# Optimization experiments

Measured on AMD Instinct MI355X. Metric: run time of the kernel, lower is better.

Reference implementation:

```python
import jax, jax.numpy as jnp
import numpy as np

S, B, D, H = 2048, 2, 1024, 16
DK = D // H  # 64
SCALE = 1.0 / np.sqrt(DK)


def setup_inputs() -> dict:
    key = jax.random.key(0)
    ks = jax.random.split(key, 12)
    std = 0.02
    return {
        "query": jax.random.normal(ks[0], (S, B, D), jnp.float32),
        "key": jax.random.normal(ks[1], (S, B, D), jnp.float32),
        "value": jax.random.normal(ks[2], (S, B, D), jnp.float32),
        "wq": jax.random.normal(ks[3], (D, D), jnp.float32) * std,
        "bq": jnp.zeros((D,), jnp.float32),
        "wk": jax.random.normal(ks[4], (D, D), jnp.float32) * std,
        "bk": jnp.zeros((D,), jnp.float32),
        "wv": jax.random.normal(ks[5], (D, D), jnp.float32) * std,
        "bv": jnp.zeros((D,), jnp.float32),
        "wo": jax.random.normal(ks[6], (D, D), jnp.float32) * std,
        "bo": jnp.zeros((D,), jnp.float32),
    }


def _proj(x, w, b):
    # (s, b, d_model) -> (s, b, heads, d_k); nn.Linear uses x @ W^T + b
    y = x @ w.T + b
    return y.reshape(*x.shape[:-1], H, DK)


def reference(query, key, value, wq, bq, wk, bk, wv, bv, wo, bo):
    q = _proj(query, wq, bq)   # (s, b, h, d)
    k = _proj(key, wk, bk)
    v = _proj(value, wv, bv)
    scores = jnp.einsum("ibhd,jbhd->ijbh", q, k) * SCALE  # (s_q, s_k, b, h)
    attn = jax.nn.softmax(scores, axis=1)  # softmax over key axis (dim=1)
    # dropout is identity in eval/reference mode
    x = jnp.einsum("ijbh,jbhd->ibhd", attn, v)  # (s, b, h, d)
    x = x.reshape(S, B, D)
    return x @ wo.T + bo
```

## Files before the change

### kernel.cpp

```cpp
#include <hip/hip_runtime.h>
#include <hip/hip_bf16.h>

namespace {

constexpr int SEQ = 2048;
constexpr int NB  = 2;
constexpr int DM  = 1024;
constexpr int NHD = 16;
constexpr int DKH = 64;
constexpr int MROWS = SEQ * NB;
constexpr float SM_SCALE = 0.125f;
constexpr size_t HT = (size_t)NB * NHD * SEQ * DKH;

typedef short bf16x8 __attribute__((ext_vector_type(8)));
typedef short bf16x4 __attribute__((ext_vector_type(4)));
typedef float f32x4  __attribute__((ext_vector_type(4)));

__device__ inline short f2bf(float f) {
    __hip_bfloat16 h = __float2bfloat16(f);
    return *reinterpret_cast<short*>(&h);
}

__device__ inline unsigned perm_pack_bf16(float hi, float lo) {
    return __builtin_amdgcn_perm(__float_as_uint(hi), __float_as_uint(lo),
                                 0x07060302u);
}

__device__ inline void gload_lds16(const short* g, short* l) {
    __builtin_amdgcn_global_load_lds(
        (const __attribute__((address_space(1))) void*)g,
        (__attribute__((address_space(3))) void*)l, 16, 0, 0);
}

__device__ inline f32x4 mfma16x16x16(bf16x4 a, bf16x4 b, f32x4 c) {
#if __has_builtin(__builtin_amdgcn_mfma_f32_16x16x16bf16_1k)
    return __builtin_amdgcn_mfma_f32_16x16x16bf16_1k(a, b, c, 0, 0, 0);
#else
    f32x4 d;
    asm("v_mfma_f32_16x16x16_bf16 %0, %1, %2, %3"
        : "=v"(d) : "v"(a), "v"(b), "v"(c));
    return d;
#endif
}

__global__ __launch_bounds__(256)
void cast3_kernel(const float* __restrict__ q, const float* __restrict__ k,
                  const float* __restrict__ v, short* __restrict__ oq,
                  short* __restrict__ ok, short* __restrict__ ov)
{
    const int t = blockIdx.x * 256 + threadIdx.x;
    const float* s = blockIdx.y == 0 ? q : blockIdx.y == 1 ? k : v;
    short* d       = blockIdx.y == 0 ? oq : blockIdx.y == 1 ? ok : ov;
    const float4 a = ((const float4*)s)[2 * t];
    const float4 b = ((const float4*)s)[2 * t + 1];
    short r[8] = {f2bf(a.x), f2bf(a.y), f2bf(a.z), f2bf(a.w),
                  f2bf(b.x), f2bf(b.y), f2bf(b.z), f2bf(b.w)};
    *(bf16x8*)(d + 8 * (size_t)t) = *(bf16x8*)r;
}

__global__ __launch_bounds__(256)
void castW_kernel(const float* __restrict__ w0, const float* __restrict__ w1,
                  const float* __restrict__ w2, const float* __restrict__ w3,
                  short* __restrict__ o)
{
    const int t = blockIdx.x * 256 + threadIdx.x;
    const float* s = blockIdx.y == 0 ? w0 : blockIdx.y == 1 ? w1
                   : blockIdx.y == 2 ? w2 : w3;
    short* d = o + (size_t)blockIdx.y * (DM * DM);
    const float4 a = ((const float4*)s)[2 * t];
    const float4 b = ((const float4*)s)[2 * t + 1];
    short r[8] = {f2bf(a.x), f2bf(a.y), f2bf(a.z), f2bf(a.w),
                  f2bf(b.x), f2bf(b.y), f2bf(b.z), f2bf(b.w)};
    *(bf16x8*)(d + 8 * (size_t)t) = *(bf16x8*)r;
}

__global__ __launch_bounds__(256)
void gemm_qkv(const short* __restrict__ X0, const short* __restrict__ X1,
              const short* __restrict__ X2, const short* __restrict__ W,
              const float* __restrict__ b0, const float* __restrict__ b1,
              const float* __restrict__ b2, short* __restrict__ Yh)
{
    __shared__ short As[128 * 64];
    __shared__ short Bs[128 * 64];
    const int tid  = threadIdx.x;
    const int lane = tid & 63;
    const int wave = tid >> 6;
    const int i16  = lane & 15;
    const int quad = lane >> 4;

    const int c    = blockIdx.y * gridDim.x + blockIdx.x;
    const int xcd  = c & 7;
    const int idx  = c >> 3;
    const int m0   = (xcd * 4 + (idx & 3)) * 128;
    const int n0g  = (idx >> 2) * 128;

    const int R0   = (wave & 1) * 64;
    const int C0   = (wave >> 1) * 64;

    const int seg = n0g >> 10;
    const short* X = seg == 0 ? X0 : seg == 1 ? X1 : X2;

    const int srow = lane >> 3;
    const int ssl  = (lane & 7) ^ srow;

    const short* ag[4]; short* al[4];
    const short* bg[4]; short* bl[4];
    #pragma unroll
    for (int i = 0; i < 4; ++i) {
        const int row = i * 32 + wave * 8 + srow;
        ag[i] = X + (size_t)(m0 + row) * DM + ssl * 8;
        al[i] = &As[i * 2048 + wave * 512];
        bg[i] = W + (size_t)(n0g + row) * DM + ssl * 8;
        bl[i] = &Bs[i * 2048 + wave * 512];
    }

    int aoff[4][2], boff[4][2];
    #pragma unroll
    for (int rt = 0; rt < 4; ++rt)
        #pragma unroll
        for (int kc = 0; kc < 2; ++kc)
            aoff[rt][kc] = (R0 + rt * 16 + i16) * 64 +
                           (((kc * 4 + quad) ^ (i16 & 7)) * 8);
    #pragma unroll
    for (int ct = 0; ct < 4; ++ct)
        #pragma unroll
        for (int kc = 0; kc < 2; ++kc)
            boff[ct][kc] = (C0 + ct * 16 + i16) * 64 +
                           (((kc * 4 + quad) ^ (i16 & 7)) * 8);

    f32x4 acc[4][4];
    #pragma unroll
    for (int rt = 0; rt < 4; ++rt)
        #pragma unroll
        for (int ct = 0; ct < 4; ++ct) acc[rt][ct] = (f32x4){0.f, 0.f, 0.f, 0.f};

    for (int ks = 0; ks < 16; ++ks) {
        __syncthreads();
        #pragma unroll
        for (int i = 0; i < 4; ++i) gload_lds16(ag[i], al[i]);
        #pragma unroll
        for (int i = 0; i < 4; ++i) gload_lds16(bg[i], bl[i]);
        __syncthreads();

        #pragma unroll
        for (int kc = 0; kc < 2; ++kc) {
            bf16x8 af[4], bfr[4];
            #pragma unroll
            for (int rt = 0; rt < 4; ++rt) af[rt] = *(const bf16x8*)&As[aoff[rt][kc]];
            #pragma unroll
            for (int ct = 0; ct < 4; ++ct) bfr[ct] = *(const bf16x8*)&Bs[boff[ct][kc]];
            #pragma unroll
            for (int rt = 0; rt < 4; ++rt)
                #pragma unroll
                for (int ct = 0; ct < 4; ++ct)
                    acc[rt][ct] = __builtin_amdgcn_mfma_f32_16x16x32_bf16(
                        af[rt], bfr[ct], acc[rt][ct], 0, 0, 0);
        }
        #pragma unroll
        for (int i = 0; i < 4; ++i) { ag[i] += 64; bg[i] += 64; }
    }

    #pragma unroll
    for (int ct = 0; ct < 4; ++ct) {
        const int n = n0g + C0 + ct * 16 + i16;
        const int nn  = n & 1023;
        const int h = nn >> 6, dk = nn & 63;
        const float* bp = seg == 0 ? b0 : seg == 1 ? b1 : b2;
        const float bb = bp[nn];
        const float sc = seg == 0 ? SM_SCALE : 1.0f;
        short* dst = Yh + (size_t)seg * HT;
        #pragma unroll
        for (int rt = 0; rt < 4; ++rt)
            #pragma unroll
            for (int r = 0; r < 4; ++r) {
                const int m = m0 + R0 + rt * 16 + quad * 4 + r;
                const int s = m >> 1, b = m & 1;
                dst[((size_t)(b * NHD + h) * SEQ + s) * DKH + dk] =
                    f2bf((acc[rt][ct][r] + bb) * sc);
            }
    }
}

__global__ __launch_bounds__(256)
void gemm_out(const short* __restrict__ X, const short* __restrict__ W,
              const float* __restrict__ bias, float* __restrict__ Y)
{
    __shared__ short As[128 * 64];
    __shared__ short Bs[64 * 64];
    const int tid  = threadIdx.x;
    const int lane = tid & 63;
    const int wave = tid >> 6;
    const int i16  = lane & 15;
    const int quad = lane >> 4;

    const int c   = blockIdx.y * gridDim.x + blockIdx.x;
    const int xcd = c & 7;
    const int idx = c >> 3;
    const int m0  = (xcd * 4 + (idx & 3)) * 128;
    const int n0  = (idx >> 2) * 64;

    const int R0   = wave * 32;

    const int srow = lane >> 3;
    const int ssl  = (lane & 7) ^ srow;

    const short* ag[4]; short* al[4];
    const short* bg[2]; short* bl[2];
    #pragma unroll
    for (int i = 0; i < 4; ++i) {
        const int row = i * 32 + wave * 8 + srow;
        ag[i] = X + (size_t)(m0 + row) * DM + ssl * 8;
        al[i] = &As[i * 2048 + wave * 512];
    }
    #pragma unroll
    for (int i = 0; i < 2; ++i) {
        const int row = i * 32 + wave * 8 + srow;
        bg[i] = W + (size_t)(n0 + row) * DM + ssl * 8;
        bl[i] = &Bs[i * 2048 + wave * 512];
    }

    int aoff[2][2], boff[4][2];
    #pragma unroll
    for (int rt = 0; rt < 2; ++rt)
        #pragma unroll
        for (int kc = 0; kc < 2; ++kc)
            aoff[rt][kc] = (R0 + rt * 16 + i16) * 64 +
                           (((kc * 4 + quad) ^ (i16 & 7)) * 8);
    #pragma unroll
    for (int ct = 0; ct < 4; ++ct)
        #pragma unroll
        for (int kc = 0; kc < 2; ++kc)
            boff[ct][kc] = (ct * 16 + i16) * 64 +
                           (((kc * 4 + quad) ^ (i16 & 7)) * 8);

    f32x4 acc[2][4];
    #pragma unroll
    for (int rt = 0; rt < 2; ++rt)
        #pragma unroll
        for (int ct = 0; ct < 4; ++ct) acc[rt][ct] = (f32x4){0.f, 0.f, 0.f, 0.f};

    for (int ks = 0; ks < 16; ++ks) {
        __syncthreads();
        #pragma unroll
        for (int i = 0; i < 4; ++i) gload_lds16(ag[i], al[i]);
        #pragma unroll
        for (int i = 0; i < 2; ++i) gload_lds16(bg[i], bl[i]);
        __syncthreads();

        #pragma unroll
        for (int kc = 0; kc < 2; ++kc) {
            bf16x8 af[2], bfr[4];
            #pragma unroll
            for (int rt = 0; rt < 2; ++rt) af[rt] = *(const bf16x8*)&As[aoff[rt][kc]];
            #pragma unroll
            for (int ct = 0; ct < 4; ++ct) bfr[ct] = *(const bf16x8*)&Bs[boff[ct][kc]];
            #pragma unroll
            for (int rt = 0; rt < 2; ++rt)
                #pragma unroll
                for (int ct = 0; ct < 4; ++ct)
                    acc[rt][ct] = __builtin_amdgcn_mfma_f32_16x16x32_bf16(
                        af[rt], bfr[ct], acc[rt][ct], 0, 0, 0);
        }
        #pragma unroll
        for (int i = 0; i < 4; ++i) ag[i] += 64;
        #pragma unroll
        for (int i = 0; i < 2; ++i) bg[i] += 64;
    }

    #pragma unroll
    for (int ct = 0; ct < 4; ++ct) {
        const int n = n0 + ct * 16 + i16;
        const float bb = bias[n];
        #pragma unroll
        for (int rt = 0; rt < 2; ++rt)
            #pragma unroll
            for (int r = 0; r < 4; ++r) {
                const int m = m0 + R0 + rt * 16 + quad * 4 + r;
                Y[(size_t)m * DM + n] = acc[rt][ct][r] + bb;
            }
    }
}

__global__ __launch_bounds__(256)
void transpose_v(const short* __restrict__ V, short* __restrict__ Vt)
{
    __shared__ alignas(16) short tile[64][72];
    const int tid = threadIdx.x;
    const int s0  = blockIdx.x * 64;
    const int bh  = blockIdx.y;
    const int row = tid >> 2;
    const int c0  = (tid & 3) * 16;

    const short* src = V + ((size_t)bh * SEQ + s0 + row) * DKH + c0;
    *(bf16x8*)&tile[row][c0]     = *(const bf16x8*)src;
    *(bf16x8*)&tile[row][c0 + 8] = *(const bf16x8*)(src + 8);
    __syncthreads();

    alignas(16) short vals[16];
    #pragma unroll
    for (int i = 0; i < 16; ++i) vals[i] = tile[c0 + i][row];
    short* dst = Vt + ((size_t)bh * DKH + row) * SEQ + s0 + c0;
    *(bf16x8*)dst       = *(bf16x8*)&vals[0];
    *(bf16x8*)(dst + 8) = *(bf16x8*)&vals[8];
}

__global__ __launch_bounds__(512)
void attn_mfma3(const short* __restrict__ Qb, const short* __restrict__ Kb,
                const short* __restrict__ Vtb, short* __restrict__ Xa)
{
    __shared__ char smem[35328];
    float* Of = (float*)smem;
    float* Ls = (float*)(smem + 34816);

    const int tid  = threadIdx.x;
    const int lane = tid & 63;
    const int wave = tid >> 6;
    const int half = wave >> 2;
    const int w4   = wave & 3;
    const int i16  = lane & 15;
    const int quad = lane >> 4;

    const int c   = blockIdx.y * gridDim.x + blockIdx.x;
    const int xcd = c & 7;
    const int idx = c >> 3;
    const int bh  = xcd * 4 + (idx >> 4);
    const int r0  = (idx & 15) * 128;

    short* Ks = (short*)(smem + half * 8192);
    short* Vs = (short*)(smem + 16384 + half * 8192);

    bf16x8 qf[2][2];
    #pragma unroll
    for (int qt = 0; qt < 2; ++qt) {
        const short* qrow =
            Qb + ((size_t)bh * SEQ + r0 + w4 * 32 + qt * 16 + i16) * DKH;
        qf[qt][0] = *(const bf16x8*)(qrow + quad * 8);
        qf[qt][1] = *(const bf16x8*)(qrow + 32 + quad * 8);
    }

    f32x4 o[2][4];
    #pragma unroll
    for (int qt = 0; qt < 2; ++qt)
        #pragma unroll
        for (int dkt = 0; dkt < 4; ++dkt) o[qt][dkt] = (f32x4){0.f, 0.f, 0.f, 0.f};
    float lsum[2] = {0.f, 0.f};

    const int srow = lane >> 3;
    const int ssl  = (lane & 7) ^ srow;
    const short* kg[2]; short* kl[2];
    const short* vg[2]; short* vl[2];
    #pragma unroll
    for (int i = 0; i < 2; ++i) {
        const int row = i * 32 + w4 * 8 + srow;
        kg[i] = Kb  + (size_t)bh * SEQ * DKH +
                (size_t)(half * 1024 + row) * DKH + ssl * 8;
        kl[i] = &Ks[i * 2048 + w4 * 512];
        vg[i] = Vtb + (size_t)bh * DKH * SEQ + (size_t)row * SEQ +
                half * 1024 + ssl * 8;
        vl[i] = &Vs[i * 2048 + w4 * 512];
    }

    int koff[4][2];
    #pragma unroll
    for (int t = 0; t < 4; ++t)
        #pragma unroll
        for (int kc = 0; kc < 2; ++kc)
            koff[t][kc] = (t * 16 + i16) * 64 +
                          (((kc * 4 + quad) ^ (i16 & 7)) * 8);
    int voff[4][4];
    #pragma unroll
    for (int jw = 0; jw < 4; ++jw)
        #pragma unroll
        for (int dkt = 0; dkt < 4; ++dkt)
            voff[jw][dkt] = (dkt * 16 + i16) * 64 +
                            (((2 * jw + (quad >> 1)) ^ (i16 & 7)) * 8) +
                            (quad & 1) * 4;

    for (int jt = 0; jt < 16; ++jt) {
        __syncthreads();
        gload_lds16(kg[0] + (size_t)jt * 64 * DKH, kl[0]);
        gload_lds16(kg[1] + (size_t)jt * 64 * DKH, kl[1]);
        gload_lds16(vg[0] + jt * 64, vl[0]);
        gload_lds16(vg[1] + jt * 64, vl[1]);
        __syncthreads();

        bf16x8 kf[4][2];
        #pragma unroll
        for (int t = 0; t < 4; ++t) {
            kf[t][0] = *(const bf16x8*)&Ks[koff[t][0]];
            kf[t][1] = *(const bf16x8*)&Ks[koff[t][1]];
        }

        bf16x4 pa[2][4];
        #pragma unroll
        for (int qt = 0; qt < 2; ++qt) {
            #pragma unroll
            for (int t = 0; t < 4; ++t) {
                f32x4 st = (f32x4){0.f, 0.f, 0.f, 0.f};
                st = __builtin_amdgcn_mfma_f32_16x16x32_bf16(kf[t][0], qf[qt][0], st, 0, 0, 0);
                st = __builtin_amdgcn_mfma_f32_16x16x32_bf16(kf[t][1], qf[qt][1], st, 0, 0, 0);
                const float e0 = __expf(st[0]);
                const float e1 = __expf(st[1]);
                const float e2 = __expf(st[2]);
                const float e3 = __expf(st[3]);
                lsum[qt] += (e0 + e1) + (e2 + e3);
                union { unsigned u[2]; bf16x4 v; } pk;
                pk.u[0] = perm_pack_bf16(e1, e0);
                pk.u[1] = perm_pack_bf16(e3, e2);
                pa[qt][t] = pk.v;
            }
        }

        #pragma unroll
        for (int jw = 0; jw < 4; ++jw) {
            #pragma unroll
            for (int dkt = 0; dkt < 4; ++dkt) {
                const bf16x4 vb = *(const bf16x4*)&Vs[voff[jw][dkt]];
                o[0][dkt] = mfma16x16x16(pa[0][jw], vb, o[0][dkt]);
                o[1][dkt] = mfma16x16x16(pa[1][jw], vb, o[1][dkt]);
            }
        }
    }

    float lred[2];
    #pragma unroll
    for (int qt = 0; qt < 2; ++qt) {
        float v = lsum[qt];
        v += __shfl_xor(v, 16, 64);
        v += __shfl_xor(v, 32, 64);
        lred[qt] = v;
    }

    __syncthreads();
    if (half == 1) {
        #pragma unroll
        for (int qt = 0; qt < 2; ++qt) {
            if (quad == 0) Ls[w4 * 32 + qt * 16 + i16] = lred[qt];
            #pragma unroll
            for (int r = 0; r < 4; ++r) {
                const int row = w4 * 32 + qt * 16 + quad * 4 + r;
                #pragma unroll
                for (int dkt = 0; dkt < 4; ++dkt)
                    Of[row * 68 + dkt * 16 + i16] = o[qt][dkt][r];
            }
        }
    }
    __syncthreads();
    if (half == 0) {
        const int b = bh / NHD;
        const int h = bh % NHD;
        float linv[2];
        #pragma unroll
        for (int qt = 0; qt < 2; ++qt)
            linv[qt] = 1.f / (lred[qt] + Ls[w4 * 32 + qt * 16 + i16]);
        #pragma unroll
        for (int qt = 0; qt < 2; ++qt) {
            #pragma unroll
            for (int r = 0; r < 4; ++r) {
                const float iv = __shfl(linv[qt], quad * 4 + r, 64);
                const int row = w4 * 32 + qt * 16 + quad * 4 + r;
                const int s = r0 + row;
                const int m = s * NB + b;
                short* op = Xa + (size_t)m * DM + h * DKH;
                #pragma unroll
                for (int dkt = 0; dkt < 4; ++dkt)
                    op[dkt * 16 + i16] =
                        f2bf((o[qt][dkt][r] + Of[row * 68 + dkt * 16 + i16]) * iv);
            }
        }
    }
}

}

extern "C" void kernel_launch(void* const* d_in, const int* in_sizes, int n_in,
                              void* d_out, int out_size, void* d_ws, size_t ws_size,
                              hipStream_t stream)
{
    const float* query = (const float*)d_in[0];
    const float* key_  = (const float*)d_in[1];
    const float* value = (const float*)d_in[2];
    const float* wq    = (const float*)d_in[3];
    const float* bq    = (const float*)d_in[4];
    const float* wk    = (const float*)d_in[5];
    const float* bk    = (const float*)d_in[6];
    const float* wv    = (const float*)d_in[7];
    const float* bv    = (const float*)d_in[8];
    const float* wo    = (const float*)d_in[9];
    const float* bo    = (const float*)d_in[10];
    float* out = (float*)d_out;

    char* ws = (char*)d_ws;
    const size_t HB = HT * sizeof(short);
    short* Qb = (short*)(ws);
    short* Kb = Qb + HT;
    short* Vb = Qb + 2 * HT;
    short* Xq = (short*)(ws + 3 * HB);
    short* Vt = Xq;
    short* Xk = (short*)(ws + 4 * HB);
    short* Xa = Xk;
    short* Xv = (short*)(ws + 5 * HB);
    short* Wb = (short*)(ws + 6 * HB);

    cast3_kernel<<<dim3(MROWS * DM / (8 * 256), 3), 256, 0, stream>>>(
        query, key_, value, Xq, Xk, Xv);
    castW_kernel<<<dim3(DM * DM / (8 * 256), 4), 256, 0, stream>>>(
        wq, wk, wv, wo, Wb);

    gemm_qkv<<<dim3(MROWS / 128, 3 * DM / 128), 256, 0, stream>>>(
        Xq, Xk, Xv, Wb, bq, bk, bv, Qb);

    transpose_v<<<dim3(SEQ / 64, NB * NHD), 256, 0, stream>>>(Vb, Vt);

    attn_mfma3<<<dim3(SEQ / 128, NB * NHD), 512, 0, stream>>>(Qb, Kb, Vt, Xa);

    gemm_out<<<dim3(MROWS / 128, DM / 64), 256, 0, stream>>>(
        Xa, Wb + 3 * (size_t)DM * DM, bo, out);
}
```

Baseline: 225.5 us.

## Double-buffer LDS in attention and out-proj, fuse V transpose and cast kernels

Merges the activation and weight cast kernels into one launch. The QKV GEMM epilogue now writes V directly in transposed layout, which removes the separate transpose kernel. The attention and output-projection kernels double-buffer their LDS tiles so the next tile's global-to-LDS load overlaps the current tile's MFMA work, with one barrier per iteration instead of two. In exchange, LDS use grows to 64KB in attention (which may lower occupancy), and the transposed V stores from the GEMM epilogue are scattered 2-byte writes.

```diff
diff --git a/kernel.cpp b/kernel.cpp
--- a/kernel.cpp
+++ b/kernel.cpp
@@ -44,41 +44,38 @@
 }
 
 __global__ __launch_bounds__(256)
-void cast3_kernel(const float* __restrict__ q, const float* __restrict__ k,
-                  const float* __restrict__ v, short* __restrict__ oq,
-                  short* __restrict__ ok, short* __restrict__ ov)
+void cast_all(const float* __restrict__ q, const float* __restrict__ k,
+              const float* __restrict__ v, const float* __restrict__ w0,
+              const float* __restrict__ w1, const float* __restrict__ w2,
+              const float* __restrict__ w3, short* __restrict__ oq,
+              short* __restrict__ ok, short* __restrict__ ov,
+              short* __restrict__ ow)
 {
-    const int t = blockIdx.x * 256 + threadIdx.x;
-    const float* s = blockIdx.y == 0 ? q : blockIdx.y == 1 ? k : v;
-    short* d       = blockIdx.y == 0 ? oq : blockIdx.y == 1 ? ok : ov;
+    const int y = blockIdx.y;
+    const float* s;
+    short* d;
+    if (y < 3) {
+        s = y == 0 ? q : y == 1 ? k : v;
+        d = y == 0 ? oq : y == 1 ? ok : ov;
+    } else {
+        if (blockIdx.x >= 512) return;
+        s = y == 3 ? w0 : y == 4 ? w1 : y == 5 ? w2 : w3;
+        d = ow + (size_t)(y - 3) * (DM * DM);
+    }
+    const size_t t = (size_t)blockIdx.x * 256 + threadIdx.x;
     const float4 a = ((const float4*)s)[2 * t];
     const float4 b = ((const float4*)s)[2 * t + 1];
     short r[8] = {f2bf(a.x), f2bf(a.y), f2bf(a.z), f2bf(a.w),
                   f2bf(b.x), f2bf(b.y), f2bf(b.z), f2bf(b.w)};
-    *(bf16x8*)(d + 8 * (size_t)t) = *(bf16x8*)r;
-}
-
-__global__ __launch_bounds__(256)
-void castW_kernel(const float* __restrict__ w0, const float* __restrict__ w1,
-                  const float* __restrict__ w2, const float* __restrict__ w3,
-                  short* __restrict__ o)
-{
-    const int t = blockIdx.x * 256 + threadIdx.x;
-    const float* s = blockIdx.y == 0 ? w0 : blockIdx.y == 1 ? w1
-                   : blockIdx.y == 2 ? w2 : w3;
-    short* d = o + (size_t)blockIdx.y * (DM * DM);
-    const float4 a = ((const float4*)s)[2 * t];
-    const float4 b = ((const float4*)s)[2 * t + 1];
-    short r[8] = {f2bf(a.x), f2bf(a.y), f2bf(a.z), f2bf(a.w),
-                  f2bf(b.x), f2bf(b.y), f2bf(b.z), f2bf(b.w)};
-    *(bf16x8*)(d + 8 * (size_t)t) = *(bf16x8*)r;
+    *(bf16x8*)(d + 8 * t) = *(bf16x8*)r;
 }
 
 __global__ __launch_bounds__(256)
 void gemm_qkv(const short* __restrict__ X0, const short* __restrict__ X1,
               const short* __restrict__ X2, const short* __restrict__ W,
               const float* __restrict__ b0, const float* __restrict__ b1,
-              const float* __restrict__ b2, short* __restrict__ Yh)
+              const float* __restrict__ b2, short* __restrict__ Qb,
+              short* __restrict__ Kb, short* __restrict__ Vt)
 {
     __shared__ short As[128 * 64];
     __shared__ short Bs[128 * 64];
@@ -168,15 +165,19 @@
         const float* bp = seg == 0 ? b0 : seg == 1 ? b1 : b2;
         const float bb = bp[nn];
         const float sc = seg == 0 ? SM_SCALE : 1.0f;
-        short* dst = Yh + (size_t)seg * HT;
         #pragma unroll
         for (int rt = 0; rt < 4; ++rt)
             #pragma unroll
             for (int r = 0; r < 4; ++r) {
                 const int m = m0 + R0 + rt * 16 + quad * 4 + r;
                 const int s = m >> 1, b = m & 1;
-                dst[((size_t)(b * NHD + h) * SEQ + s) * DKH + dk] =
-                    f2bf((acc[rt][ct][r] + bb) * sc);
+                const short val = f2bf((acc[rt][ct][r] + bb) * sc);
+                if (seg == 2) {
+                    Vt[(((size_t)(b * NHD + h) * DKH + dk) << 11) + s] = val;
+                } else {
+                    short* dst = seg == 0 ? Qb : Kb;
+                    dst[((size_t)(b * NHD + h) * SEQ + s) * DKH + dk] = val;
+                }
             }
     }
 }
@@ -185,8 +186,7 @@
 void gemm_out(const short* __restrict__ X, const short* __restrict__ W,
               const float* __restrict__ bias, float* __restrict__ Y)
 {
-    __shared__ short As[128 * 64];
-    __shared__ short Bs[64 * 64];
+    __shared__ short sAB[2][12288];
     const int tid  = threadIdx.x;
     const int lane = tid & 63;
     const int wave = tid >> 6;
@@ -204,19 +204,19 @@
     const int srow = lane >> 3;
     const int ssl  = (lane & 7) ^ srow;
 
-    const short* ag[4]; short* al[4];
-    const short* bg[2]; short* bl[2];
+    const short* ag[4]; int alo[4];
+    const short* bg[2]; int blo[2];
     #pragma unroll
     for (int i = 0; i < 4; ++i) {
         const int row = i * 32 + wave * 8 + srow;
         ag[i] = X + (size_t)(m0 + row) * DM + ssl * 8;
-        al[i] = &As[i * 2048 + wave * 512];
+        alo[i] = i * 2048 + wave * 512;
     }
     #pragma unroll
     for (int i = 0; i < 2; ++i) {
         const int row = i * 32 + wave * 8 + srow;
         bg[i] = W + (size_t)(n0 + row) * DM + ssl * 8;
-        bl[i] = &Bs[i * 2048 + wave * 512];
+        blo[i] = 8192 + i * 2048 + wave * 512;
     }
 
     int aoff[2][2], boff[4][2];
@@ -230,7 +230,7 @@
     for (int ct = 0; ct < 4; ++ct)
         #pragma unroll
         for (int kc = 0; kc < 2; ++kc)
-            boff[ct][kc] = (ct * 16 + i16) * 64 +
+            boff[ct][kc] = 8192 + (ct * 16 + i16) * 64 +
                            (((kc * 4 + quad) ^ (i16 & 7)) * 8);
 
     f32x4 acc[2][4];
@@ -239,21 +239,36 @@
         #pragma unroll
         for (int ct = 0; ct < 4; ++ct) acc[rt][ct] = (f32x4){0.f, 0.f, 0.f, 0.f};
 
+    #pragma unroll
+    for (int i = 0; i < 4; ++i) gload_lds16(ag[i], &sAB[0][alo[i]]);
+    #pragma unroll
+    for (int i = 0; i < 2; ++i) gload_lds16(bg[i], &sAB[0][blo[i]]);
+    #pragma unroll
+    for (int i = 0; i < 4; ++i) ag[i] += 64;
+    #pragma unroll
+    for (int i = 0; i < 2; ++i) bg[i] += 64;
+    __syncthreads();
+
     for (int ks = 0; ks < 16; ++ks) {
-        __syncthreads();
-        #pragma unroll
-        for (int i = 0; i < 4; ++i) gload_lds16(ag[i], al[i]);
-        #pragma unroll
-        for (int i = 0; i < 2; ++i) gload_lds16(bg[i], bl[i]);
-        __syncthreads();
-
+        const int p = ks & 1;
+        if (ks < 15) {
+            #pragma unroll
+            for (int i = 0; i < 4; ++i) gload_lds16(ag[i], &sAB[1 - p][alo[i]]);
+            #pragma unroll
+            for (int i = 0; i < 2; ++i) gload_lds16(bg[i], &sAB[1 - p][blo[i]]);
+            #pragma unroll
+            for (int i = 0; i < 4; ++i) ag[i] += 64;
+            #pragma unroll
+            for (int i = 0; i < 2; ++i) bg[i] += 64;
+        }
+        const short* buf = sAB[p];
         #pragma unroll
         for (int kc = 0; kc < 2; ++kc) {
             bf16x8 af[2], bfr[4];
             #pragma unroll
-            for (int rt = 0; rt < 2; ++rt) af[rt] = *(const bf16x8*)&As[aoff[rt][kc]];
-            #pragma unroll
-            for (int ct = 0; ct < 4; ++ct) bfr[ct] = *(const bf16x8*)&Bs[boff[ct][kc]];
+            for (int rt = 0; rt < 2; ++rt) af[rt] = *(const bf16x8*)&buf[aoff[rt][kc]];
+            #pragma unroll
+            for (int ct = 0; ct < 4; ++ct) bfr[ct] = *(const bf16x8*)&buf[boff[ct][kc]];
             #pragma unroll
             for (int rt = 0; rt < 2; ++rt)
                 #pragma unroll
@@ -261,10 +276,7 @@
                     acc[rt][ct] = __builtin_amdgcn_mfma_f32_16x16x32_bf16(
                         af[rt], bfr[ct], acc[rt][ct], 0, 0, 0);
         }
-        #pragma unroll
-        for (int i = 0; i < 4; ++i) ag[i] += 64;
-        #pragma unroll
-        for (int i = 0; i < 2; ++i) bg[i] += 64;
+        __syncthreads();
     }
 
     #pragma unroll
@@ -281,36 +293,13 @@
     }
 }
 
-__global__ __launch_bounds__(256)
-void transpose_v(const short* __restrict__ V, short* __restrict__ Vt)
-{
-    __shared__ alignas(16) short tile[64][72];
-    const int tid = threadIdx.x;
-    const int s0  = blockIdx.x * 64;
-    const int bh  = blockIdx.y;
-    const int row = tid >> 2;
-    const int c0  = (tid & 3) * 16;
-
-    const short* src = V + ((size_t)bh * SEQ + s0 + row) * DKH + c0;
-    *(bf16x8*)&tile[row][c0]     = *(const bf16x8*)src;
-    *(bf16x8*)&tile[row][c0 + 8] = *(const bf16x8*)(src + 8);
-    __syncthreads();
-
-    alignas(16) short vals[16];
-    #pragma unroll
-    for (int i = 0; i < 16; ++i) vals[i] = tile[c0 + i][row];
-    short* dst = Vt + ((size_t)bh * DKH + row) * SEQ + s0 + c0;
-    *(bf16x8*)dst       = *(bf16x8*)&vals[0];
-    *(bf16x8*)(dst + 8) = *(bf16x8*)&vals[8];
-}
-
 __global__ __launch_bounds__(512)
-void attn_mfma3(const short* __restrict__ Qb, const short* __restrict__ Kb,
+void attn_mfma4(const short* __restrict__ Qb, const short* __restrict__ Kb,
                 const short* __restrict__ Vtb, short* __restrict__ Xa)
 {
-    __shared__ char smem[35328];
-    float* Of = (float*)smem;
-    float* Ls = (float*)(smem + 34816);
+    __shared__ short sm[32768];
+    float* Of = (float*)sm;
+    float* Ls = (float*)((char*)sm + 34816);
 
     const int tid  = threadIdx.x;
     const int lane = tid & 63;
@@ -326,9 +315,6 @@
     const int bh  = xcd * 4 + (idx >> 4);
     const int r0  = (idx & 15) * 128;
 
-    short* Ks = (short*)(smem + half * 8192);
-    short* Vs = (short*)(smem + 16384 + half * 8192);
-
     bf16x8 qf[2][2];
     #pragma unroll
     for (int qt = 0; qt < 2; ++qt) {
@@ -347,17 +333,17 @@
 
     const int srow = lane >> 3;
     const int ssl  = (lane & 7) ^ srow;
-    const short* kg[2]; short* kl[2];
-    const short* vg[2]; short* vl[2];
+    const short* kg[2]; const short* vg[2];
+    int kls[2], vls[2];
     #pragma unroll
     for (int i = 0; i < 2; ++i) {
         const int row = i * 32 + w4 * 8 + srow;
         kg[i] = Kb  + (size_t)bh * SEQ * DKH +
                 (size_t)(half * 1024 + row) * DKH + ssl * 8;
-        kl[i] = &Ks[i * 2048 + w4 * 512];
+        kls[i] = half * 4096 + i * 2048 + w4 * 512;
         vg[i] = Vtb + (size_t)bh * DKH * SEQ + (size_t)row * SEQ +
                 half * 1024 + ssl * 8;
-        vl[i] = &Vs[i * 2048 + w4 * 512];
+        vls[i] = 8192 + half * 4096 + i * 2048 + w4 * 512;
     }
 
     int koff[4][2];
@@ -365,30 +351,39 @@
     for (int t = 0; t < 4; ++t)
         #pragma unroll
         for (int kc = 0; kc < 2; ++kc)
-            koff[t][kc] = (t * 16 + i16) * 64 +
+            koff[t][kc] = half * 4096 + (t * 16 + i16) * 64 +
                           (((kc * 4 + quad) ^ (i16 & 7)) * 8);
     int voff[4][4];
     #pragma unroll
     for (int jw = 0; jw < 4; ++jw)
         #pragma unroll
         for (int dkt = 0; dkt < 4; ++dkt)
-            voff[jw][dkt] = (dkt * 16 + i16) * 64 +
+            voff[jw][dkt] = 8192 + half * 4096 + (dkt * 16 + i16) * 64 +
                             (((2 * jw + (quad >> 1)) ^ (i16 & 7)) * 8) +
                             (quad & 1) * 4;
 
+    gload_lds16(kg[0], &sm[kls[0]]);
+    gload_lds16(kg[1], &sm[kls[1]]);
+    gload_lds16(vg[0], &sm[vls[0]]);
+    gload_lds16(vg[1], &sm[vls[1]]);
+    __syncthreads();
+
     for (int jt = 0; jt < 16; ++jt) {
-        __syncthreads();
-        gload_lds16(kg[0] + (size_t)jt * 64 * DKH, kl[0]);
-        gload_lds16(kg[1] + (size_t)jt * 64 * DKH, kl[1]);
-        gload_lds16(vg[0] + jt * 64, vl[0]);
-        gload_lds16(vg[1] + jt * 64, vl[1]);
-        __syncthreads();
+        const int p = jt & 1;
+        if (jt < 15) {
+            const int bo = (1 - p) * 16384;
+            gload_lds16(kg[0] + (size_t)(jt + 1) * 64 * DKH, &sm[bo + kls[0]]);
+            gload_lds16(kg[1] + (size_t)(jt + 1) * 64 * DKH, &sm[bo + kls[1]]);
+            gload_lds16(vg[0] + (jt + 1) * 64, &sm[bo + vls[0]]);
+            gload_lds16(vg[1] + (jt + 1) * 64, &sm[bo + vls[1]]);
+        }
+        const short* buf = sm + p * 16384;
 
         bf16x8 kf[4][2];
         #pragma unroll
         for (int t = 0; t < 4; ++t) {
-            kf[t][0] = *(const bf16x8*)&Ks[koff[t][0]];
-            kf[t][1] = *(const bf16x8*)&Ks[koff[t][1]];
+            kf[t][0] = *(const bf16x8*)&buf[koff[t][0]];
+            kf[t][1] = *(const bf16x8*)&buf[koff[t][1]];
         }
 
         bf16x4 pa[2][4];
@@ -415,11 +410,12 @@
         for (int jw = 0; jw < 4; ++jw) {
             #pragma unroll
             for (int dkt = 0; dkt < 4; ++dkt) {
-                const bf16x4 vb = *(const bf16x4*)&Vs[voff[jw][dkt]];
+                const bf16x4 vb = *(const bf16x4*)&buf[voff[jw][dkt]];
                 o[0][dkt] = mfma16x16x16(pa[0][jw], vb, o[0][dkt]);
                 o[1][dkt] = mfma16x16x16(pa[1][jw], vb, o[1][dkt]);
             }
         }
+        __syncthreads();
     }
 
     float lred[2];
@@ -431,7 +427,6 @@
         lred[qt] = v;
     }
 
-    __syncthreads();
     if (half == 1) {
         #pragma unroll
         for (int qt = 0; qt < 2; ++qt) {
@@ -494,25 +489,20 @@
     const size_t HB = HT * sizeof(short);
     short* Qb = (short*)(ws);
     short* Kb = Qb + HT;
-    short* Vb = Qb + 2 * HT;
+    short* Vt = Qb + 2 * HT;
     short* Xq = (short*)(ws + 3 * HB);
-    short* Vt = Xq;
+    short* Xa = Xq;
     short* Xk = (short*)(ws + 4 * HB);
-    short* Xa = Xk;
     short* Xv = (short*)(ws + 5 * HB);
     short* Wb = (short*)(ws + 6 * HB);
 
-    cast3_kernel<<<dim3(MROWS * DM / (8 * 256), 3), 256, 0, stream>>>(
-        query, key_, value, Xq, Xk, Xv);
-    castW_kernel<<<dim3(DM * DM / (8 * 256), 4), 256, 0, stream>>>(
-        wq, wk, wv, wo, Wb);
+    cast_all<<<dim3(MROWS * DM / (8 * 256), 7), 256, 0, stream>>>(
+        query, key_, value, wq, wk, wv, wo, Xq, Xk, Xv, Wb);
 
     gemm_qkv<<<dim3(MROWS / 128, 3 * DM / 128), 256, 0, stream>>>(
-        Xq, Xk, Xv, Wb, bq, bk, bv, Qb);
-
-    transpose_v<<<dim3(SEQ / 64, NB * NHD), 256, 0, stream>>>(Vb, Vt);
-
-    attn_mfma3<<<dim3(SEQ / 128, NB * NHD), 512, 0, stream>>>(Qb, Kb, Vt, Xa);
+        Xq, Xk, Xv, Wb, bq, bk, bv, Qb, Kb, Vt);
+
+    attn_mfma4<<<dim3(SEQ / 128, NB * NHD), 512, 0, stream>>>(Qb, Kb, Vt, Xa);
 
     gemm_out<<<dim3(MROWS / 128, DM / 64), 256, 0, stream>>>(
         Xa, Wb + 3 * (size_t)DM * DM, bo, out);
```

New measurement: 220.6 us. 1.02x faster.
